# Optimization experiments

Measured on AMD Instinct MI355X. Metric: run time of the kernel, lower is better.

The kernel has to match this reference:

```python
import jax, jax.numpy as jnp
import numpy as np

EPS = 0.1        # entropic regularization (init eps)
MAX_ITER = 30    # init max_iter
THRESH = 0.1     # hardcoded convergence threshold in the module


def setup_inputs() -> dict:
    key = jax.random.key(0)
    k1, k2, k3, k4 = jax.random.split(key, 4)
    N, P, D = 4, 1024, 32
    return {
        "x": jax.random.normal(k1, (N, P, D), dtype=jnp.float32),
        "y": jax.random.normal(k2, (N, P, D), dtype=jnp.float32),
        "x_weights": jax.random.uniform(k3, (N, P), dtype=jnp.float32),
        "y_weights": jax.random.uniform(k4, (N, P), dtype=jnp.float32),
    }


def _sinkhorn(x, y, x_weights, y_weights):
    # Squared-Euclidean cost matrix |x_i - y_j|^2 -> (N, P1, P2)
    x2 = jnp.sum(x * x, axis=-1)
    y2 = jnp.sum(y * y, axis=-1)
    C = x2[..., :, None] + y2[..., None, :] - 2.0 * jnp.einsum("npd,nqd->npq", x, y)

    # mu/nu are detached in the original (requires_grad_(False)); normalized by GLOBAL sum
    mu = jax.lax.stop_gradient(x_weights / jnp.sum(x_weights))
    nu = jax.lax.stop_gradient(y_weights / jnp.sum(y_weights))
    log_mu = jnp.log(mu + 1e-8)
    log_nu = jnp.log(nu + 1e-8)

    def M(u, v):  # (-C + u_i + v_j) / eps
        return (-C + u[..., :, None] + v[..., None, :]) / EPS

    def step(carry, _):
        u, v, done = carry
        u_new = EPS * (log_mu - jax.scipy.special.logsumexp(M(u, v), axis=-1)) + u
        v_new = EPS * (log_nu - jax.scipy.special.logsumexp(M(u_new, v), axis=-2)) + v
        err = jnp.mean(jnp.sum(jnp.abs(u_new - u), axis=-1))
        # Once converged (early break in the torch loop), freeze u/v
        u = jnp.where(done, u, u_new)
        v = jnp.where(done, v, v_new)
        done = done | (err < THRESH)
        return (u, v, done), None

    u0 = jnp.zeros_like(mu)
    v0 = jnp.zeros_like(nu)
    (u, v, _), _ = jax.lax.scan(step, (u0, v0, jnp.array(False)), None, length=MAX_ITER)

    pi = jnp.exp(M(u, v))                      # transport plan (N, P1, P2)
    cost = jnp.sum(pi * C, axis=(-2, -1))      # (N,)  (reduction='none')
    return cost


def reference(x, y, x_weights, y_weights):
    return _sinkhorn(x, y, x_weights, y_weights)
```

## Files before the change

### kernel.cpp

```cpp
#include <hip/hip_runtime.h>
#include <math.h>

#define NB    4
#define PP    1024
#define DD    32
#define MAXIT 30
#define PBLK  1024
#define BTHR  256

__device__ float  g_C [NB*PP*PP];
__device__ float  g_Ct[NB*PP*PP];
__device__ float  g_logmu[NB*PP], g_lognu[NB*PP];
__device__ float  g_u[NB*PP], g_v[NB*PP];
__device__ double g_errpart[MAXIT*PBLK];
__device__ int    g_done[MAXIT+1];
__device__ double g_costpart[PBLK];

__global__ __launch_bounds__(BTHR)
void prep_kernel(const float* __restrict__ xw, const float* __restrict__ yw)
{
    const int t = threadIdx.x, lane = t & 63, wid = t >> 6;
    double sx = 0.0, sy = 0.0;
    for (int i = t; i < NB*PP; i += BTHR) { sx += (double)xw[i]; sy += (double)yw[i]; }
#pragma unroll
    for (int o = 32; o > 0; o >>= 1) { sx += __shfl_xor(sx, o); sy += __shfl_xor(sy, o); }
    __shared__ double a[4], b[4];
    if (lane == 0) { a[wid] = sx; b[wid] = sy; }
    __syncthreads();
    const double Sx = ((a[0]+a[1])+a[2])+a[3];
    const double Sy = ((b[0]+b[1])+b[2])+b[3];
    for (int i = t; i < NB*PP; i += BTHR) {
        g_logmu[i] = (float)log((double)xw[i]/Sx + 1e-8);
        g_lognu[i] = (float)log((double)yw[i]/Sy + 1e-8);
        g_u[i] = 0.f;
        g_v[i] = 0.f;
    }
    if (t <= MAXIT) g_done[t] = 0;
}

__global__ __launch_bounds__(BTHR)
void build_kernel(const float* __restrict__ x, const float* __restrict__ y)
{
    const int t = threadIdx.x;
    const int bid = blockIdx.x;
    const bool isC = bid < 512;
    const int b = isC ? bid : bid - 512;
    const int n = b >> 7;
    const int nbase = n << 10;
    const int gr0 = b << 3;

    __shared__ float rows[8][DD];
    {
        const int r = t >> 5, d = t & 31;
        const float* src = isC ? x : y;
        rows[r][d] = src[(gr0 + r) * DD + d];
    }
    __syncthreads();

    const float* other = isC ? y : x;
    float* dst = isC ? g_C : g_Ct;

    const float4* op0 = reinterpret_cast<const float4*>(other + ((size_t)(nbase + t      ) << 5));
    const float4* op1 = reinterpret_cast<const float4*>(other + ((size_t)(nbase + t + 256) << 5));
    const float4* op2 = reinterpret_cast<const float4*>(other + ((size_t)(nbase + t + 512) << 5));
    const float4* op3 = reinterpret_cast<const float4*>(other + ((size_t)(nbase + t + 768) << 5));

    float acc0[8], acc1[8], acc2[8], acc3[8];
#pragma unroll
    for (int r = 0; r < 8; ++r) { acc0[r] = 0.f; acc1[r] = 0.f; acc2[r] = 0.f; acc3[r] = 0.f; }

#pragma unroll
    for (int j = 0; j < 8; ++j) {
        const float4 f0 = op0[j];
        const float4 f1 = op1[j];
        const float4 f2 = op2[j];
        const float4 f3 = op3[j];
#pragma unroll
        for (int r = 0; r < 8; ++r) {
            const float4 rv = *reinterpret_cast<const float4*>(&rows[r][4*j]);
            float d;
            d = rv.x - f0.x; acc0[r] = fmaf(d, d, acc0[r]);
            d = rv.y - f0.y; acc0[r] = fmaf(d, d, acc0[r]);
            d = rv.z - f0.z; acc0[r] = fmaf(d, d, acc0[r]);
            d = rv.w - f0.w; acc0[r] = fmaf(d, d, acc0[r]);
            d = rv.x - f1.x; acc1[r] = fmaf(d, d, acc1[r]);
            d = rv.y - f1.y; acc1[r] = fmaf(d, d, acc1[r]);
            d = rv.z - f1.z; acc1[r] = fmaf(d, d, acc1[r]);
            d = rv.w - f1.w; acc1[r] = fmaf(d, d, acc1[r]);
            d = rv.x - f2.x; acc2[r] = fmaf(d, d, acc2[r]);
            d = rv.y - f2.y; acc2[r] = fmaf(d, d, acc2[r]);
            d = rv.z - f2.z; acc2[r] = fmaf(d, d, acc2[r]);
            d = rv.w - f2.w; acc2[r] = fmaf(d, d, acc2[r]);
            d = rv.x - f3.x; acc3[r] = fmaf(d, d, acc3[r]);
            d = rv.y - f3.y; acc3[r] = fmaf(d, d, acc3[r]);
            d = rv.z - f3.z; acc3[r] = fmaf(d, d, acc3[r]);
            d = rv.w - f3.w; acc3[r] = fmaf(d, d, acc3[r]);
        }
    }
#pragma unroll
    for (int r = 0; r < 8; ++r) {
        float* row = dst + (((size_t)(gr0 + r)) << 10);
        row[t      ] = acc0[r];
        row[t + 256] = acc1[r];
        row[t + 512] = acc2[r];
        row[t + 768] = acc3[r];
    }
}

__global__ __launch_bounds__(BTHR)
void u_kernel(int it)
{
    const int t = threadIdx.x, lane = t & 63, wid = t >> 6;
    const int b = blockIdx.x;
    const int n = b >> 8;
    const int nbase = n << 10;
    const int done = g_done[it];
    const int gr = (b << 2) + wid;

    const float4* Vp = reinterpret_cast<const float4*>(g_v + nbase);
    const float4* Cp = reinterpret_cast<const float4*>(g_C + ((size_t)gr << 10));

    float tv[16];
    float mx = -1e30f;
#pragma unroll
    for (int k = 0; k < 4; ++k) {
        const float4 cf = Cp[lane + (k << 6)];
        const float4 vf = Vp[lane + (k << 6)];
        tv[4*k+0] = (vf.x - cf.x) * 10.f;
        tv[4*k+1] = (vf.y - cf.y) * 10.f;
        tv[4*k+2] = (vf.z - cf.z) * 10.f;
        tv[4*k+3] = (vf.w - cf.w) * 10.f;
    }
#pragma unroll
    for (int i = 0; i < 16; ++i) mx = fmaxf(mx, tv[i]);
#pragma unroll
    for (int o = 32; o > 0; o >>= 1) mx = fmaxf(mx, __shfl_xor(mx, o));
    float s = 0.f;
#pragma unroll
    for (int i = 0; i < 16; ++i) s += __expf(tv[i] - mx);
#pragma unroll
    for (int o = 32; o > 0; o >>= 1) s += __shfl_xor(s, o);
    const float lse  = mx + __logf(s);
    const float unew = 0.1f * (g_logmu[gr] - lse);

    __shared__ double dred[4];
    if (lane == 0) {
        dred[wid] = fabs((double)unew - (double)g_u[gr]);
        if (!done) g_u[gr] = unew;
    }
    __syncthreads();
    if (t == 0) g_errpart[it * PBLK + b] = ((dred[0]+dred[1])+dred[2])+dred[3];
}

__global__ __launch_bounds__(BTHR)
void v_kernel(int it)
{
    const int t = threadIdx.x, lane = t & 63, wid = t >> 6;
    const int b = blockIdx.x;
    const int n = b >> 8;
    const int nbase = n << 10;
    const int done = g_done[it];

    if (b == 0) {
        const double* p = g_errpart + it * PBLK;
        double s = ((p[t] + p[t+256]) + p[t+512]) + p[t+768];
#pragma unroll
        for (int o = 32; o > 0; o >>= 1) s += __shfl_xor(s, o);
        __shared__ double sred[4];
        if (lane == 0) sred[wid] = s;
        __syncthreads();
        if (t == 0) {
            const double tot = ((sred[0]+sred[1])+sred[2])+sred[3];
            g_done[it + 1] = done | (tot < 0.4);
        }
    }

    const int gr = (b << 2) + wid;
    const float4* Up = reinterpret_cast<const float4*>(g_u + nbase);
    const float4* Cp = reinterpret_cast<const float4*>(g_Ct + ((size_t)gr << 10));

    float tv[16];
    float mx = -1e30f;
#pragma unroll
    for (int k = 0; k < 4; ++k) {
        const float4 cf = Cp[lane + (k << 6)];
        const float4 uf = Up[lane + (k << 6)];
        tv[4*k+0] = (uf.x - cf.x) * 10.f;
        tv[4*k+1] = (uf.y - cf.y) * 10.f;
        tv[4*k+2] = (uf.z - cf.z) * 10.f;
        tv[4*k+3] = (uf.w - cf.w) * 10.f;
    }
#pragma unroll
    for (int i = 0; i < 16; ++i) mx = fmaxf(mx, tv[i]);
#pragma unroll
    for (int o = 32; o > 0; o >>= 1) mx = fmaxf(mx, __shfl_xor(mx, o));
    float s = 0.f;
#pragma unroll
    for (int i = 0; i < 16; ++i) s += __expf(tv[i] - mx);
#pragma unroll
    for (int o = 32; o > 0; o >>= 1) s += __shfl_xor(s, o);
    const float lse  = mx + __logf(s);
    const float vnew = 0.1f * (g_lognu[gr] - lse);
    if (lane == 0 && !done) g_v[gr] = vnew;
}

__global__ __launch_bounds__(BTHR)
void cost_kernel()
{
    const int t = threadIdx.x, lane = t & 63, wid = t >> 6;
    const int b = blockIdx.x;
    const int n = b >> 8;
    const int nbase = n << 10;
    const int gr = (b << 2) + wid;

    const float4* Vp = reinterpret_cast<const float4*>(g_v + nbase);
    const float4* Cp = reinterpret_cast<const float4*>(g_C + ((size_t)gr << 10));
    const float ur = g_u[gr];

    double part = 0.0;
#pragma unroll
    for (int k = 0; k < 4; ++k) {
        const float4 cf = Cp[lane + (k << 6)];
        const float4 vf = Vp[lane + (k << 6)];
        part += (double)__expf((ur + vf.x - cf.x) * 10.f) * (double)cf.x;
        part += (double)__expf((ur + vf.y - cf.y) * 10.f) * (double)cf.y;
        part += (double)__expf((ur + vf.z - cf.z) * 10.f) * (double)cf.z;
        part += (double)__expf((ur + vf.w - cf.w) * 10.f) * (double)cf.w;
    }
#pragma unroll
    for (int o = 32; o > 0; o >>= 1) part += __shfl_xor(part, o);
    __shared__ double red[4];
    if (lane == 0) red[wid] = part;
    __syncthreads();
    if (t == 0) g_costpart[b] = ((red[0]+red[1])+red[2])+red[3];
}

__global__ __launch_bounds__(64)
void out_kernel(float* __restrict__ out)
{
    const int t = threadIdx.x;
#pragma unroll 1
    for (int n = 0; n < NB; ++n) {
        const double* cp = g_costpart + (n << 8);
        double s = ((cp[t] + cp[t+64]) + cp[t+128]) + cp[t+192];
#pragma unroll
        for (int o = 32; o > 0; o >>= 1) s += __shfl_xor(s, o);
        if (t == 0) out[n] = (float)s;
    }
}

extern "C" void kernel_launch(void* const* d_in, const int* in_sizes, int n_in,
                              void* d_out, int out_size, void* d_ws, size_t ws_size,
                              hipStream_t stream)
{
    (void)in_sizes; (void)n_in; (void)out_size; (void)d_ws; (void)ws_size;
    const float* x  = (const float*)d_in[0];
    const float* y  = (const float*)d_in[1];
    const float* xw = (const float*)d_in[2];
    const float* yw = (const float*)d_in[3];
    float* out = (float*)d_out;

    hipLaunchKernelGGL(prep_kernel,  dim3(1),    dim3(BTHR), 0, stream, xw, yw);
    hipLaunchKernelGGL(build_kernel, dim3(1024), dim3(BTHR), 0, stream, x, y);
    for (int it = 0; it < MAXIT; ++it) {
        hipLaunchKernelGGL(u_kernel, dim3(PBLK), dim3(BTHR), 0, stream, it);
        hipLaunchKernelGGL(v_kernel, dim3(PBLK), dim3(BTHR), 0, stream, it);
    }
    hipLaunchKernelGGL(cost_kernel, dim3(PBLK), dim3(BTHR), 0, stream);
    hipLaunchKernelGGL(out_kernel,  dim3(1),    dim3(64),   0, stream, out);
}
```

Baseline: 338.2 us.

## Fuse column logsumexp partials into u pass and drop transposed cost matrix

Removes the transposed cost matrix. The u-update kernel now also emits per-block column partial (max, sum) pairs for the v logsumexp, computed from the freshly updated u and the same C rows already held in registers. A small combine kernel then merges 128 partials per column with an online logsumexp to produce v. This halves cost-matrix memory traffic per iteration and the build work, at the price of an extra partial buffer write/read and a very small 16-block combine kernel that may be latency-bound.

```diff
diff --git a/kernel.cpp b/kernel.cpp
--- a/kernel.cpp
+++ b/kernel.cpp
@@ -5,16 +5,16 @@
 #define PP    1024
 #define DD    32
 #define MAXIT 30
-#define PBLK  1024
+#define MBLK  512
 #define BTHR  256
 
-__device__ float  g_C [NB*PP*PP];
-__device__ float  g_Ct[NB*PP*PP];
+__device__ float  g_C[NB*PP*PP];
 __device__ float  g_logmu[NB*PP], g_lognu[NB*PP];
 __device__ float  g_u[NB*PP], g_v[NB*PP];
-__device__ double g_errpart[MAXIT*PBLK];
+__device__ float2 g_pms[MBLK*PP];
+__device__ double g_errpart[MAXIT*MBLK];
 __device__ int    g_done[MAXIT+1];
-__device__ double g_costpart[PBLK];
+__device__ double g_costpart[1024];
 
 __global__ __launch_bounds__(BTHR)
 void prep_kernel(const float* __restrict__ xw, const float* __restrict__ yw)
@@ -42,9 +42,7 @@
 void build_kernel(const float* __restrict__ x, const float* __restrict__ y)
 {
     const int t = threadIdx.x;
-    const int bid = blockIdx.x;
-    const bool isC = bid < 512;
-    const int b = isC ? bid : bid - 512;
+    const int b = blockIdx.x;
     const int n = b >> 7;
     const int nbase = n << 10;
     const int gr0 = b << 3;
@@ -52,54 +50,47 @@
     __shared__ float rows[8][DD];
     {
         const int r = t >> 5, d = t & 31;
-        const float* src = isC ? x : y;
-        rows[r][d] = src[(gr0 + r) * DD + d];
+        rows[r][d] = x[(gr0 + r) * DD + d];
     }
     __syncthreads();
 
-    const float* other = isC ? y : x;
-    float* dst = isC ? g_C : g_Ct;
-
-    const float4* op0 = reinterpret_cast<const float4*>(other + ((size_t)(nbase + t      ) << 5));
-    const float4* op1 = reinterpret_cast<const float4*>(other + ((size_t)(nbase + t + 256) << 5));
-    const float4* op2 = reinterpret_cast<const float4*>(other + ((size_t)(nbase + t + 512) << 5));
-    const float4* op3 = reinterpret_cast<const float4*>(other + ((size_t)(nbase + t + 768) << 5));
+    const float4* op0 = reinterpret_cast<const float4*>(y + ((size_t)(nbase + t      ) << 5));
+    const float4* op1 = reinterpret_cast<const float4*>(y + ((size_t)(nbase + t + 256) << 5));
+    const float4* op2 = reinterpret_cast<const float4*>(y + ((size_t)(nbase + t + 512) << 5));
+    const float4* op3 = reinterpret_cast<const float4*>(y + ((size_t)(nbase + t + 768) << 5));
 
     float acc0[8], acc1[8], acc2[8], acc3[8];
 #pragma unroll
-    for (int r = 0; r < 8; ++r) { acc0[r] = 0.f; acc1[r] = 0.f; acc2[r] = 0.f; acc3[r] = 0.f; }
+    for (int r = 0; r < 8; ++r) { acc0[r]=0.f; acc1[r]=0.f; acc2[r]=0.f; acc3[r]=0.f; }
 
 #pragma unroll
     for (int j = 0; j < 8; ++j) {
-        const float4 f0 = op0[j];
-        const float4 f1 = op1[j];
-        const float4 f2 = op2[j];
-        const float4 f3 = op3[j];
+        const float4 f0 = op0[j], f1 = op1[j], f2 = op2[j], f3 = op3[j];
 #pragma unroll
         for (int r = 0; r < 8; ++r) {
             const float4 rv = *reinterpret_cast<const float4*>(&rows[r][4*j]);
             float d;
-            d = rv.x - f0.x; acc0[r] = fmaf(d, d, acc0[r]);
-            d = rv.y - f0.y; acc0[r] = fmaf(d, d, acc0[r]);
-            d = rv.z - f0.z; acc0[r] = fmaf(d, d, acc0[r]);
-            d = rv.w - f0.w; acc0[r] = fmaf(d, d, acc0[r]);
-            d = rv.x - f1.x; acc1[r] = fmaf(d, d, acc1[r]);
-            d = rv.y - f1.y; acc1[r] = fmaf(d, d, acc1[r]);
-            d = rv.z - f1.z; acc1[r] = fmaf(d, d, acc1[r]);
-            d = rv.w - f1.w; acc1[r] = fmaf(d, d, acc1[r]);
-            d = rv.x - f2.x; acc2[r] = fmaf(d, d, acc2[r]);
-            d = rv.y - f2.y; acc2[r] = fmaf(d, d, acc2[r]);
-            d = rv.z - f2.z; acc2[r] = fmaf(d, d, acc2[r]);
-            d = rv.w - f2.w; acc2[r] = fmaf(d, d, acc2[r]);
-            d = rv.x - f3.x; acc3[r] = fmaf(d, d, acc3[r]);
-            d = rv.y - f3.y; acc3[r] = fmaf(d, d, acc3[r]);
-            d = rv.z - f3.z; acc3[r] = fmaf(d, d, acc3[r]);
-            d = rv.w - f3.w; acc3[r] = fmaf(d, d, acc3[r]);
+            d = rv.x-f0.x; acc0[r]=fmaf(d,d,acc0[r]);
+            d = rv.y-f0.y; acc0[r]=fmaf(d,d,acc0[r]);
+            d = rv.z-f0.z; acc0[r]=fmaf(d,d,acc0[r]);
+            d = rv.w-f0.w; acc0[r]=fmaf(d,d,acc0[r]);
+            d = rv.x-f1.x; acc1[r]=fmaf(d,d,acc1[r]);
+            d = rv.y-f1.y; acc1[r]=fmaf(d,d,acc1[r]);
+            d = rv.z-f1.z; acc1[r]=fmaf(d,d,acc1[r]);
+            d = rv.w-f1.w; acc1[r]=fmaf(d,d,acc1[r]);
+            d = rv.x-f2.x; acc2[r]=fmaf(d,d,acc2[r]);
+            d = rv.y-f2.y; acc2[r]=fmaf(d,d,acc2[r]);
+            d = rv.z-f2.z; acc2[r]=fmaf(d,d,acc2[r]);
+            d = rv.w-f2.w; acc2[r]=fmaf(d,d,acc2[r]);
+            d = rv.x-f3.x; acc3[r]=fmaf(d,d,acc3[r]);
+            d = rv.y-f3.y; acc3[r]=fmaf(d,d,acc3[r]);
+            d = rv.z-f3.z; acc3[r]=fmaf(d,d,acc3[r]);
+            d = rv.w-f3.w; acc3[r]=fmaf(d,d,acc3[r]);
         }
     }
 #pragma unroll
     for (int r = 0; r < 8; ++r) {
-        float* row = dst + (((size_t)(gr0 + r)) << 10);
+        float* row = g_C + (((size_t)(gr0 + r)) << 10);
         row[t      ] = acc0[r];
         row[t + 256] = acc1[r];
         row[t + 512] = acc2[r];
@@ -108,66 +99,114 @@
 }
 
 __global__ __launch_bounds__(BTHR)
-void u_kernel(int it)
+void main_kernel(int it)
 {
     const int t = threadIdx.x, lane = t & 63, wid = t >> 6;
     const int b = blockIdx.x;
-    const int n = b >> 8;
+    const int n = b >> 7;
     const int nbase = n << 10;
     const int done = g_done[it];
-    const int gr = (b << 2) + wid;
+    const int gr0 = (b << 3) + (wid << 1);
+
+    __shared__ float2 lpm[4][PP];
+    __shared__ double dred[4];
 
     const float4* Vp = reinterpret_cast<const float4*>(g_v + nbase);
-    const float4* Cp = reinterpret_cast<const float4*>(g_C + ((size_t)gr << 10));
-
-    float tv[16];
-    float mx = -1e30f;
+    float vv[16];
+    {
+#pragma unroll
+        for (int k = 0; k < 4; ++k) {
+            const float4 f = Vp[lane + (k << 6)];
+            vv[4*k+0]=f.x; vv[4*k+1]=f.y; vv[4*k+2]=f.z; vv[4*k+3]=f.w;
+        }
+    }
+    float c0[16], c1[16];
+    {
+        const float4* C0 = reinterpret_cast<const float4*>(g_C + ((size_t)gr0 << 10));
+        const float4* C1 = reinterpret_cast<const float4*>(g_C + ((size_t)(gr0+1) << 10));
+#pragma unroll
+        for (int k = 0; k < 4; ++k) {
+            float4 f = C0[lane + (k << 6)];
+            c0[4*k+0]=f.x; c0[4*k+1]=f.y; c0[4*k+2]=f.z; c0[4*k+3]=f.w;
+            f = C1[lane + (k << 6)];
+            c1[4*k+0]=f.x; c1[4*k+1]=f.y; c1[4*k+2]=f.z; c1[4*k+3]=f.w;
+        }
+    }
+
+    float tv0[16], tv1[16];
+    float mx0 = -1e30f, mx1 = -1e30f;
+#pragma unroll
+    for (int i = 0; i < 16; ++i) {
+        tv0[i] = (vv[i] - c0[i]) * 10.f;  mx0 = fmaxf(mx0, tv0[i]);
+        tv1[i] = (vv[i] - c1[i]) * 10.f;  mx1 = fmaxf(mx1, tv1[i]);
+    }
+#pragma unroll
+    for (int o = 32; o > 0; o >>= 1) {
+        mx0 = fmaxf(mx0, __shfl_xor(mx0, o));
+        mx1 = fmaxf(mx1, __shfl_xor(mx1, o));
+    }
+    float s0 = 0.f, s1 = 0.f;
+#pragma unroll
+    for (int i = 0; i < 16; ++i) {
+        s0 += __expf(tv0[i] - mx0);
+        s1 += __expf(tv1[i] - mx1);
+    }
+#pragma unroll
+    for (int o = 32; o > 0; o >>= 1) {
+        s0 += __shfl_xor(s0, o);
+        s1 += __shfl_xor(s1, o);
+    }
+    const float un0 = 0.1f * (g_logmu[gr0]   - (mx0 + __logf(s0)));
+    const float un1 = 0.1f * (g_logmu[gr0+1] - (mx1 + __logf(s1)));
+    const float uo0 = g_u[gr0], uo1 = g_u[gr0+1];
+    const float uc0 = done ? uo0 : un0;
+    const float uc1 = done ? uo1 : un1;
+    if (lane == 0) {
+        if (!done) { g_u[gr0] = un0; g_u[gr0+1] = un1; }
+        dred[wid] = fabs((double)un0 - (double)uo0) + fabs((double)un1 - (double)uo1);
+    }
+
 #pragma unroll
     for (int k = 0; k < 4; ++k) {
-        const float4 cf = Cp[lane + (k << 6)];
-        const float4 vf = Vp[lane + (k << 6)];
-        tv[4*k+0] = (vf.x - cf.x) * 10.f;
-        tv[4*k+1] = (vf.y - cf.y) * 10.f;
-        tv[4*k+2] = (vf.z - cf.z) * 10.f;
-        tv[4*k+3] = (vf.w - cf.w) * 10.f;
-    }
-#pragma unroll
-    for (int i = 0; i < 16; ++i) mx = fmaxf(mx, tv[i]);
-#pragma unroll
-    for (int o = 32; o > 0; o >>= 1) mx = fmaxf(mx, __shfl_xor(mx, o));
-    float s = 0.f;
-#pragma unroll
-    for (int i = 0; i < 16; ++i) s += __expf(tv[i] - mx);
-#pragma unroll
-    for (int o = 32; o > 0; o >>= 1) s += __shfl_xor(s, o);
-    const float lse  = mx + __logf(s);
-    const float unew = 0.1f * (g_logmu[gr] - lse);
-
-    __shared__ double dred[4];
-    if (lane == 0) {
-        dred[wid] = fabs((double)unew - (double)g_u[gr]);
-        if (!done) g_u[gr] = unew;
+#pragma unroll
+        for (int j = 0; j < 4; ++j) {
+            const int i = 4*k + j;
+            const float a0 = (uc0 - c0[i]) * 10.f;
+            const float a1 = (uc1 - c1[i]) * 10.f;
+            const float m  = fmaxf(a0, a1);
+            const float s  = __expf(a0 - m) + __expf(a1 - m);
+            lpm[wid][4*(lane + (k << 6)) + j] = make_float2(m, s);
+        }
     }
     __syncthreads();
-    if (t == 0) g_errpart[it * PBLK + b] = ((dred[0]+dred[1])+dred[2])+dred[3];
-}
-
-__global__ __launch_bounds__(BTHR)
-void v_kernel(int it)
-{
-    const int t = threadIdx.x, lane = t & 63, wid = t >> 6;
-    const int b = blockIdx.x;
-    const int n = b >> 8;
-    const int nbase = n << 10;
+
+    if (t == 0) g_errpart[(size_t)it * MBLK + b] = ((dred[0]+dred[1])+dred[2])+dred[3];
+#pragma unroll
+    for (int c = 0; c < 4; ++c) {
+        const int q = t + (c << 8);
+        const float2 a = lpm[0][q], b2 = lpm[1][q], c2 = lpm[2][q], d2 = lpm[3][q];
+        const float M = fmaxf(fmaxf(a.x, b2.x), fmaxf(c2.x, d2.x));
+        const float S = a.y*__expf(a.x-M) + b2.y*__expf(b2.x-M)
+                      + c2.y*__expf(c2.x-M) + d2.y*__expf(d2.x-M);
+        g_pms[((size_t)b << 10) + q] = make_float2(M, S);
+    }
+}
+
+__global__ __launch_bounds__(BTHR)
+void combine_kernel(int it)
+{
+    const int t = threadIdx.x;
+    const int g = (blockIdx.x << 8) + t;
+    const int n = g >> 10, q = g & 1023;
     const int done = g_done[it];
 
-    if (b == 0) {
-        const double* p = g_errpart + it * PBLK;
-        double s = ((p[t] + p[t+256]) + p[t+512]) + p[t+768];
+    if (blockIdx.x == 0) {
+        const double* p = g_errpart + (size_t)it * MBLK;
+        double s = p[t] + p[t + 256];
 #pragma unroll
         for (int o = 32; o > 0; o >>= 1) s += __shfl_xor(s, o);
         __shared__ double sred[4];
-        if (lane == 0) sred[wid] = s;
+        if ((t & 63) == 0) sred[t >> 6] = s;
         __syncthreads();
         if (t == 0) {
             const double tot = ((sred[0]+sred[1])+sred[2])+sred[3];
@@ -175,33 +214,25 @@
         }
     }
 
-    const int gr = (b << 2) + wid;
-    const float4* Up = reinterpret_cast<const float4*>(g_u + nbase);
-    const float4* Cp = reinterpret_cast<const float4*>(g_Ct + ((size_t)gr << 10));
-
-    float tv[16];
-    float mx = -1e30f;
-#pragma unroll
-    for (int k = 0; k < 4; ++k) {
-        const float4 cf = Cp[lane + (k << 6)];
-        const float4 uf = Up[lane + (k << 6)];
-        tv[4*k+0] = (uf.x - cf.x) * 10.f;
-        tv[4*k+1] = (uf.y - cf.y) * 10.f;
-        tv[4*k+2] = (uf.z - cf.z) * 10.f;
-        tv[4*k+3] = (uf.w - cf.w) * 10.f;
-    }
-#pragma unroll
-    for (int i = 0; i < 16; ++i) mx = fmaxf(mx, tv[i]);
-#pragma unroll
-    for (int o = 32; o > 0; o >>= 1) mx = fmaxf(mx, __shfl_xor(mx, o));
-    float s = 0.f;
-#pragma unroll
-    for (int i = 0; i < 16; ++i) s += __expf(tv[i] - mx);
-#pragma unroll
-    for (int o = 32; o > 0; o >>= 1) s += __shfl_xor(s, o);
-    const float lse  = mx + __logf(s);
-    const float vnew = 0.1f * (g_lognu[gr] - lse);
-    if (lane == 0 && !done) g_v[gr] = vnew;
+    const float2* P = g_pms + ((size_t)n << 17) + q;
+    float M0=-1e30f,M1=-1e30f,M2=-1e30f,M3=-1e30f;
+    float S0=0.f,S1=0.f,S2=0.f,S3=0.f;
+#pragma unroll 4
+    for (int bb = 0; bb < 128; bb += 4) {
+        const float2 p0 = P[(size_t)(bb+0) << 10];
+        const float2 p1 = P[(size_t)(bb+1) << 10];
+        const float2 p2 = P[(size_t)(bb+2) << 10];
+        const float2 p3 = P[(size_t)(bb+3) << 10];
+        float nm;
+        nm = fmaxf(M0, p0.x); S0 = S0*__expf(M0-nm) + p0.y*__expf(p0.x-nm); M0 = nm;
+        nm = fmaxf(M1, p1.x); S1 = S1*__expf(M1-nm) + p1.y*__expf(p1.x-nm); M1 = nm;
+        nm = fmaxf(M2, p2.x); S2 = S2*__expf(M2-nm) + p2.y*__expf(p2.x-nm); M2 = nm;
+        nm = fmaxf(M3, p3.x); S3 = S3*__expf(M3-nm) + p3.y*__expf(p3.x-nm); M3 = nm;
+    }
+    const float M = fmaxf(fmaxf(M0, M1), fmaxf(M2, M3));
+    const float S = S0*__expf(M0-M) + S1*__expf(M1-M) + S2*__expf(M2-M) + S3*__expf(M3-M);
+    const float vnew = 0.1f * (g_lognu[g] - (M + __logf(S)));
+    if (!done) g_v[g] = vnew;
 }
 
 __global__ __launch_bounds__(BTHR)
@@ -261,11 +292,11 @@
     float* out = (float*)d_out;
 
     hipLaunchKernelGGL(prep_kernel,  dim3(1),    dim3(BTHR), 0, stream, xw, yw);
-    hipLaunchKernelGGL(build_kernel, dim3(1024), dim3(BTHR), 0, stream, x, y);
+    hipLaunchKernelGGL(build_kernel, dim3(MBLK), dim3(BTHR), 0, stream, x, y);
     for (int it = 0; it < MAXIT; ++it) {
-        hipLaunchKernelGGL(u_kernel, dim3(PBLK), dim3(BTHR), 0, stream, it);
-        hipLaunchKernelGGL(v_kernel, dim3(PBLK), dim3(BTHR), 0, stream, it);
-    }
-    hipLaunchKernelGGL(cost_kernel, dim3(PBLK), dim3(BTHR), 0, stream);
+        hipLaunchKernelGGL(main_kernel,    dim3(MBLK), dim3(BTHR), 0, stream, it);
+        hipLaunchKernelGGL(combine_kernel, dim3(16),   dim3(BTHR), 0, stream, it);
+    }
+    hipLaunchKernelGGL(cost_kernel, dim3(1024), dim3(BTHR), 0, stream);
     hipLaunchKernelGGL(out_kernel,  dim3(1),    dim3(64),   0, stream, out);
 }
```

Result: slower. 631.1 us (+86.6%).
